# Kernel tuning notes

Measured on AMD Instinct MI355X. Metric: run time of the kernel, lower is better.

Reference implementation:

```python
import jax, jax.numpy as jnp
import numpy as np

NUM_LEVELS = 8
CODEBOOK_SIZE = 1024
EMBED_DIM = 256
BETA = 0.25
N_TOKENS = 65536
EPS = 1e-6


def setup_inputs() -> dict:
    key = jax.random.key(0)
    kz, kc = jax.random.split(key)
    z = jax.random.normal(kz, (N_TOKENS, EMBED_DIM), dtype=jnp.float32)
    # per-level init std = 1 / 2**i, matching nn.init.normal_ in __init__
    scales = (0.5 ** jnp.arange(NUM_LEVELS, dtype=jnp.float32))[:, None, None]
    codebooks = jax.random.normal(kc, (NUM_LEVELS, CODEBOOK_SIZE, EMBED_DIM), dtype=jnp.float32) * scales
    return {"z": z, "codebooks": codebooks}


def _normalize(v):
    # F.normalize(p=2, dim=-1, eps=1e-6): v / max(||v||, eps)
    return v / jnp.maximum(jnp.linalg.norm(v, axis=-1, keepdims=True), EPS)


def _rotation_trick(x, quantized):
    sg = jax.lax.stop_gradient
    u = _normalize(x)
    q = _normalize(quantized)
    w = _normalize(u + q)
    xw_dot = jnp.sum(x * sg(w), axis=-1, keepdims=True)
    xu_dot = jnp.sum(x * sg(u), axis=-1, keepdims=True)
    return x - 2.0 * xw_dot * sg(w) + 2.0 * xu_dot * sg(q)


def reference(z, codebooks):
    sg = jax.lax.stop_gradient
    residual = z
    quantized_sum = jnp.zeros_like(z)
    indices_list = []
    total_codebook_loss = jnp.float32(0.0)
    total_commitment_loss = jnp.float32(0.0)
    for lvl in range(NUM_LEVELS):
        c = codebooks[lvl]  # [K, D]
        # squared-euclidean distances up to constant ||x||^2 (argmin-equivalent, as in source)
        c_sq = jnp.sum(c * c, axis=1)                      # [K]
        dists = c_sq - 2.0 * (residual @ c.T)              # [N, K]
        min_idx = jnp.argmin(dists, axis=-1)               # [N]
        indices_list.append(min_idx)
        z_q_local = c[min_idx]                             # gather [N, D]
        total_codebook_loss = total_codebook_loss + jnp.mean((z_q_local - sg(residual)) ** 2)
        total_commitment_loss = total_commitment_loss + jnp.mean((sg(z_q_local) - residual) ** 2)
        # training path uses the rotation-trick estimator
        z_q_st = _rotation_trick(residual, z_q_local)
        residual = residual - z_q_st
        quantized_sum = quantized_sum + z_q_local
    indices = jnp.stack(indices_list, axis=-1)             # [N, L]
    loss = total_codebook_loss + BETA * total_commitment_loss
    # perplexity (codebook utilization entropy)
    flat = indices.reshape(-1)
    counts = jnp.zeros((CODEBOOK_SIZE,), jnp.float32).at[flat].add(1.0)
    probs = counts / jnp.float32(flat.size)
    safe = jnp.where(probs > 0, probs, 1.0)
    entropy = -jnp.sum(probs * jnp.log(safe))
    perplexity = jnp.exp(entropy)
    # straight-through output
    z_q = z + sg(quantized_sum - z)
    return (z_q, indices, loss, total_codebook_loss, total_commitment_loss, perplexity)
```

## Files before the change

### kernel.cpp

```cpp
#include <hip/hip_runtime.h>

#define N_TOK 65536
#define DIM 256
#define KCB 1024
#define NLVL 8
#define TPB 64
#define ND_OUT (N_TOK * DIM)
#define IDX_OFF ND_OUT
#define SC_OFF (ND_OUT + N_TOK * NLVL)
#define EPSV 1e-6f

typedef _Float16 half8 __attribute__((ext_vector_type(8)));
typedef float f32x4 __attribute__((ext_vector_type(4)));

__device__ __forceinline__ float wave_red(float v) {
    v += __shfl_xor(v, 32, 64);
    v += __shfl_xor(v, 16, 64);
    v += __shfl_xor(v, 8, 64);
    v += __shfl_xor(v, 4, 64);
    v += __shfl_xor(v, 2, 64);
    v += __shfl_xor(v, 1, 64);
    return v;
}

__device__ __forceinline__ unsigned int ordf(float d) {
    unsigned int u = __float_as_uint(d);
    return (u & 0x80000000u) ? ~u : (u ^ 0x80000000u);
}

__global__ __launch_bounds__(256) void k_prep(const float* __restrict__ cbs,
                                              half8* __restrict__ ws_b) {
    const int lvl = blockIdx.x >> 6, ntg = blockIdx.x & 63;
    const int lane = threadIdx.x & 63, sg = threadIdx.x >> 6;
    const float sc = (float)(1 << (lvl + 5));
#pragma unroll
    for (int ss = 0; ss < 2; ++ss) {
        const int s = sg + ss * 4;
        const int code = ntg * 16 + (lane & 15);
        const int d0 = s * 32 + (lane >> 4) * 8;
        const float* p = cbs + ((size_t)(lvl * KCB + code)) * DIM + d0;
        const float4 va = *(const float4*)p;
        const float4 vb = *(const float4*)(p + 4);
        float f[8] = {va.x, va.y, va.z, va.w, vb.x, vb.y, vb.z, vb.w};
        half8 h, l;
#pragma unroll
        for (int j = 0; j < 8; ++j) {
            float fs = f[j] * sc;
            _Float16 hh = (_Float16)fs;
            h[j] = hh;
            l[j] = (_Float16)(fs - (float)hh);
        }
        const size_t base = ((size_t)((lvl * 8 + s) * 64 + ntg)) * 128;
        ws_b[base + lane] = h;
        ws_b[base + 64 + lane] = l;
    }
}

__global__ __launch_bounds__(256) void k_csq(const float* __restrict__ cbs,
                                             float* __restrict__ csq_s,
                                             int* __restrict__ gcounts,
                                             float* __restrict__ gloss) {
    const int tid = threadIdx.x;
    const int wv = tid >> 6, lane = tid & 63;
    const int code = blockIdx.x * 4 + wv;
    const float4 v = *(const float4*)(cbs + (size_t)code * DIM + lane * 4);
    float s = v.x * v.x + v.y * v.y + v.z * v.z + v.w * v.w;
    s = wave_red(s);
    const int lvl = code >> 10;
    if (lane == 0) csq_s[code] = s * (float)(1 << (10 + lvl));
    if (blockIdx.x == 0) {
#pragma unroll
        for (int i = 0; i < 4; ++i) gcounts[tid + i * 256] = 0;
        if (tid == 0) *gloss = 0.f;
    }
}

__global__ __launch_bounds__(512, 2) void k_main(const float* __restrict__ z,
                                                 const float* __restrict__ cbs,
                                                 const half8* __restrict__ ws_b,
                                                 const float* __restrict__ csq_s,
                                                 float* __restrict__ out,
                                                 int* __restrict__ gcounts,
                                                 float* __restrict__ gloss) {
    __shared__ __align__(16) float Rld[TPB * DIM];
    __shared__ unsigned long long keyBuf[8][TPB];
    __shared__ int bestI_sh[TPB];
    __shared__ int idxBuf[TPB * NLVL];
    __shared__ int hist[KCB];
    __shared__ float wpart[8];

    const int tid = threadIdx.x;
    const int lane = tid & 63, w = tid >> 6;
    const int l15 = lane & 15, qd = lane >> 4;
    const int t0 = blockIdx.x * TPB;

#pragma unroll
    for (int i = 0; i < 8; ++i) {
        int fi = tid + i * 512;
        int t = fi >> 6, k4 = fi & 63;
        float4 v = *(const float4*)(z + (size_t)(t0 + t) * DIM + k4 * 4);
        v.x *= 32.f; v.y *= 32.f; v.z *= 32.f; v.w *= 32.f;
        *(float4*)&Rld[t * DIM + ((k4 ^ (t & 15)) << 2)] = v;
    }
#pragma unroll
    for (int i = 0; i < 2; ++i) hist[tid + i * 512] = 0;
    float loss_acc = 0.f;

    const half8* pbw = ws_b + (size_t)(w * 8) * 128 + lane;
    half8 bh = pbw[0], bl = pbw[64];
    __syncthreads();

    for (int lvl = 0; lvl < NLVL; ++lvl) {
        float bd[16];
        int bi[16];
#pragma unroll
        for (int i = 0; i < 16; ++i) { bd[i] = 3.402823466e38f; bi[i] = 0; }

        f32x4 acc[8][4];
#pragma unroll
        for (int nt = 0; nt < 8; ++nt)
#pragma unroll
            for (int m = 0; m < 4; ++m) acc[nt][m] = (f32x4){0.f, 0.f, 0.f, 0.f};

#pragma unroll 1
        for (int s = 0; s < 8; ++s) {
            half8 Ah[4], Al[4];
#pragma unroll
            for (int m = 0; m < 4; ++m) {
                const int row = (m * 16 + l15) * DIM;
                const int k4 = 8 * s + 2 * qd;
                float4 va = *(const float4*)&Rld[row + ((k4 ^ l15) << 2)];
                float4 vb = *(const float4*)&Rld[row + (((k4 + 1) ^ l15) << 2)];
                float f[8] = {va.x, va.y, va.z, va.w, vb.x, vb.y, vb.z, vb.w};
                half8 h, l;
#pragma unroll
                for (int j = 0; j < 8; ++j) {
                    _Float16 hh = (_Float16)f[j];
                    h[j] = hh;
                    l[j] = (_Float16)(f[j] - (float)hh);
                }
                Ah[m] = h;
                Al[m] = l;
            }
            const half8* pb = ws_b + (((size_t)(lvl * 8 + s)) * 64 + w * 8) * 128 + lane;
#pragma unroll
            for (int nt = 0; nt < 8; ++nt) {
                const int off = (nt < 7) ? (nt + 1) * 128 : 64 * 128;
                half8 nbh = pb[off];
                half8 nbl = pb[off + 64];
#pragma unroll
                for (int m = 0; m < 4; ++m)
                    acc[nt][m] = __builtin_amdgcn_mfma_f32_16x16x32_f16(Ah[m], bh, acc[nt][m], 0, 0, 0);
#pragma unroll
                for (int m = 0; m < 4; ++m)
                    acc[nt][m] = __builtin_amdgcn_mfma_f32_16x16x32_f16(Al[m], bh, acc[nt][m], 0, 0, 0);
#pragma unroll
                for (int m = 0; m < 4; ++m)
                    acc[nt][m] = __builtin_amdgcn_mfma_f32_16x16x32_f16(Ah[m], bl, acc[nt][m], 0, 0, 0);
#pragma unroll
                for (int m = 0; m < 4; ++m)
                    acc[nt][m] = __builtin_amdgcn_mfma_f32_16x16x32_f16(Al[m], bl, acc[nt][m], 0, 0, 0);
                bh = nbh;
                bl = nbl;
            }
        }
        {
            const float* csqp = csq_s + lvl * KCB + w * 128 + l15;
#pragma unroll
            for (int nt = 0; nt < 8; ++nt) {
                const float cs = csqp[nt * 16];
                const int code = w * 128 + nt * 16 + l15;
#pragma unroll
                for (int m = 0; m < 4; ++m)
#pragma unroll
                    for (int i = 0; i < 4; ++i) {
                        float d = fmaf(-2.f, acc[nt][m][i], cs);
                        if (d < bd[m * 4 + i]) { bd[m * 4 + i] = d; bi[m * 4 + i] = code; }
                    }
            }
        }
        unsigned long long key[16];
#pragma unroll
        for (int i = 0; i < 16; ++i)
            key[i] = (((unsigned long long)ordf(bd[i])) << 10) | (unsigned long long)bi[i];
#pragma unroll
        for (int m = 1; m <= 8; m <<= 1)
#pragma unroll
            for (int i = 0; i < 16; ++i) {
                unsigned long long o = __shfl_xor(key[i], m, 64);
                if (o < key[i]) key[i] = o;
            }
        if (l15 == 0) {
#pragma unroll
            for (int m = 0; m < 4; ++m)
#pragma unroll
                for (int i = 0; i < 4; ++i)
                    keyBuf[w][m * 16 + qd * 4 + i] = key[m * 4 + i];
        }
        __syncthreads();
        if (tid < TPB) {
            unsigned long long k = keyBuf[0][tid];
#pragma unroll
            for (int ww = 1; ww < 8; ++ww)
                if (keyBuf[ww][tid] < k) k = keyBuf[ww][tid];
            const int idx = (int)(k & 1023ull);
            bestI_sh[tid] = idx;
            idxBuf[tid * NLVL + lvl] = idx;
            atomicAdd(&hist[idx], 1);
        }
        __syncthreads();

        const float* cb = cbs + (size_t)lvl * KCB * DIM;
        for (int s2 = 0; s2 < 8; ++s2) {
            const int tl = w * 8 + s2;
            const int idx = bestI_sh[tl];
            const int e = tl & 15;
            float4 r4 = *(const float4*)&Rld[tl * DIM + ((lane ^ e) << 2)];
            r4.x *= 0.03125f; r4.y *= 0.03125f; r4.z *= 0.03125f; r4.w *= 0.03125f;
            float4 c4 = *(const float4*)(cb + (size_t)idx * DIM + lane * 4);
            float rr = r4.x * r4.x + r4.y * r4.y + r4.z * r4.z + r4.w * r4.w;
            float cc = c4.x * c4.x + c4.y * c4.y + c4.z * c4.z + c4.w * c4.w;
            float e0 = (c4.x - r4.x) * (c4.x - r4.x) + (c4.y - r4.y) * (c4.y - r4.y) +
                       (c4.z - r4.z) * (c4.z - r4.z) + (c4.w - r4.w) * (c4.w - r4.w);
            rr = wave_red(rr);
            cc = wave_red(cc);
            e0 = wave_red(e0);
            const float dx = fmaxf(sqrtf(rr), EPSV);
            const float dc = fmaxf(sqrtf(cc), EPSV);
            float4 u4 = make_float4(r4.x / dx, r4.y / dx, r4.z / dx, r4.w / dx);
            float4 q4 = make_float4(c4.x / dc, c4.y / dc, c4.z / dc, c4.w / dc);
            float4 w4 = make_float4(u4.x + q4.x, u4.y + q4.y, u4.z + q4.z, u4.w + q4.w);
            float ww = w4.x * w4.x + w4.y * w4.y + w4.z * w4.z + w4.w * w4.w;
            float xw = r4.x * w4.x + r4.y * w4.y + r4.z * w4.z + r4.w * w4.w;
            float xu = r4.x * u4.x + r4.y * u4.y + r4.z * u4.z + r4.w * u4.w;
            ww = wave_red(ww);
            xw = wave_red(xw);
            xu = wave_red(xu);
            const float dw = fmaxf(sqrtf(ww), EPSV);
            const float xwn = xw / dw;
            float4 wn = make_float4(w4.x / dw, w4.y / dw, w4.z / dw, w4.w / dw);
            float4 zst = make_float4(r4.x - 2.f * xwn * wn.x + 2.f * xu * q4.x,
                                     r4.y - 2.f * xwn * wn.y + 2.f * xu * q4.y,
                                     r4.z - 2.f * xwn * wn.z + 2.f * xu * q4.z,
                                     r4.w - 2.f * xwn * wn.w + 2.f * xu * q4.w);
            float4 rn = make_float4((r4.x - zst.x) * 32.f, (r4.y - zst.y) * 32.f,
                                    (r4.z - zst.z) * 32.f, (r4.w - zst.w) * 32.f);
            *(float4*)&Rld[tl * DIM + ((lane ^ e) << 2)] = rn;
            loss_acc += e0;
        }
        __syncthreads();
    }

    for (int s2 = 0; s2 < 8; ++s2) {
        const int tl = w * 8 + s2;
        const size_t trow = t0 + tl;
        float4 z4 = *(const float4*)(z + trow * DIM + lane * 4);
        float4 qs = make_float4(0.f, 0.f, 0.f, 0.f);
#pragma unroll
        for (int lvl = 0; lvl < NLVL; ++lvl) {
            const int idx = idxBuf[tl * NLVL + lvl];
            float4 c4 = *(const float4*)(cbs + ((size_t)(lvl * KCB + idx)) * DIM + lane * 4);
            qs.x += c4.x; qs.y += c4.y; qs.z += c4.z; qs.w += c4.w;
        }
        float4 o = make_float4(z4.x + (qs.x - z4.x), z4.y + (qs.y - z4.y),
                               z4.z + (qs.z - z4.z), z4.w + (qs.w - z4.w));
        *(float4*)(out + trow * DIM + lane * 4) = o;
    }
    out[IDX_OFF + (size_t)(t0 + (tid >> 3)) * NLVL + (tid & 7)] = (float)idxBuf[tid];
#pragma unroll
    for (int i = 0; i < 2; ++i) {
        int b = tid + i * 512;
        int h = hist[b];
        if (h) atomicAdd(&gcounts[b], h);
    }
    if (lane == 0) wpart[w] = loss_acc;
    __syncthreads();
    if (tid == 0) {
        float sum = 0.f;
#pragma unroll
        for (int i = 0; i < 8; ++i) sum += wpart[i];
        atomicAdd(gloss, sum);
    }
}

__global__ __launch_bounds__(256) void k_fin(const int* __restrict__ gcounts,
                                             const float* __restrict__ gloss,
                                             float* __restrict__ out) {
    __shared__ float part[4];
    const int tid = threadIdx.x, lane = tid & 63, wv = tid >> 6;
    float e = 0.f;
#pragma unroll
    for (int i = 0; i < 4; ++i) {
        float c = (float)gcounts[tid * 4 + i];
        float p = c * (1.f / 524288.f);
        if (p > 0.f) e += p * logf(p);
    }
    e = wave_red(e);
    if (lane == 0) part[wv] = e;
    __syncthreads();
    if (tid == 0) {
        float ent = -(part[0] + part[1] + part[2] + part[3]);
        float cbl = *gloss * (1.f / 16777216.f);
        out[SC_OFF + 0] = cbl + 0.25f * cbl;
        out[SC_OFF + 1] = cbl;
        out[SC_OFF + 2] = cbl;
        out[SC_OFF + 3] = expf(ent);
    }
}

extern "C" void kernel_launch(void* const* d_in, const int* in_sizes, int n_in,
                              void* d_out, int out_size, void* d_ws, size_t ws_size,
                              hipStream_t stream) {
    (void)in_sizes; (void)n_in; (void)out_size; (void)ws_size;
    const float* z = (const float*)d_in[0];
    const float* cbs = (const float*)d_in[1];
    float* out = (float*)d_out;
    half8* ws_b = (half8*)d_ws;
    float* csq = (float*)((char*)d_ws + (8u << 20));
    int* gcounts = (int*)((char*)d_ws + (8u << 20) + 32768);
    float* gloss = (float*)((char*)d_ws + (8u << 20) + 32768 + 4096);

    hipLaunchKernelGGL(k_prep, dim3(512), dim3(256), 0, stream, cbs, ws_b);
    hipLaunchKernelGGL(k_csq, dim3(2048), dim3(256), 0, stream, cbs, csq, gcounts, gloss);
    hipLaunchKernelGGL(k_main, dim3(1024), dim3(512), 0, stream, z, cbs, ws_b, csq, out,
                       gcounts, gloss);
    hipLaunchKernelGGL(k_fin, dim3(1), dim3(256), 0, stream, gcounts, gloss, out);
}
```

Measured before the change: 1.355 ms.

## Precompute split-fp16 A fragments in LDS once per level and use per-wave argmin reduce

Each level now converts the residual tile into hi/lo fp16 MFMA fragments once into shared memory, instead of every wave redoing the conversion in the inner loop. The cross-wave argmin reduction is done per wave via shuffles, removing a barrier and the bestI buffer. This cuts redundant VALU conversion work and one sync. In exchange it adds 64KB of LDS, which may reduce blocks per CU, and an extra barrier before the matmul.

```diff
diff --git a/kernel.cpp b/kernel.cpp
--- a/kernel.cpp
+++ b/kernel.cpp
@@ -83,8 +83,8 @@
                                                  int* __restrict__ gcounts,
                                                  float* __restrict__ gloss) {
     __shared__ __align__(16) float Rld[TPB * DIM];
-    __shared__ unsigned long long keyBuf[8][TPB];
-    __shared__ int bestI_sh[TPB];
+    __shared__ __align__(16) half8 Afrag[4096];
+    __shared__ unsigned long long keyBuf[8][TPB + 1];
     __shared__ int idxBuf[TPB * NLVL];
     __shared__ int hist[KCB];
     __shared__ float wpart[8];
@@ -111,6 +111,29 @@
     __syncthreads();
 
     for (int lvl = 0; lvl < NLVL; ++lvl) {
+#pragma unroll
+        for (int i = 0; i < 4; ++i) {
+            const int f = tid + i * 512;
+            const int sm = f >> 6, ln = f & 63;
+            const int s = sm >> 2, m = sm & 3;
+            const int e = ln & 15;
+            const int row = (m * 16 + e) * DIM;
+            const int k4 = s * 8 + ((ln >> 4) << 1);
+            float4 va = *(const float4*)&Rld[row + ((k4 ^ e) << 2)];
+            float4 vb = *(const float4*)&Rld[row + (((k4 + 1) ^ e) << 2)];
+            float fv[8] = {va.x, va.y, va.z, va.w, vb.x, vb.y, vb.z, vb.w};
+            half8 h, l;
+#pragma unroll
+            for (int j = 0; j < 8; ++j) {
+                _Float16 hh = (_Float16)fv[j];
+                h[j] = hh;
+                l[j] = (_Float16)(fv[j] - (float)hh);
+            }
+            Afrag[sm * 128 + ln] = h;
+            Afrag[sm * 128 + 64 + ln] = l;
+        }
+        __syncthreads();
+
         float bd[16];
         int bi[16];
 #pragma unroll
@@ -127,20 +150,8 @@
             half8 Ah[4], Al[4];
 #pragma unroll
             for (int m = 0; m < 4; ++m) {
-                const int row = (m * 16 + l15) * DIM;
-                const int k4 = 8 * s + 2 * qd;
-                float4 va = *(const float4*)&Rld[row + ((k4 ^ l15) << 2)];
-                float4 vb = *(const float4*)&Rld[row + (((k4 + 1) ^ l15) << 2)];
-                float f[8] = {va.x, va.y, va.z, va.w, vb.x, vb.y, vb.z, vb.w};
-                half8 h, l;
-#pragma unroll
-                for (int j = 0; j < 8; ++j) {
-                    _Float16 hh = (_Float16)f[j];
-                    h[j] = hh;
-                    l[j] = (_Float16)(f[j] - (float)hh);
-                }
-                Ah[m] = h;
-                Al[m] = l;
+                Ah[m] = Afrag[(s * 4 + m) * 128 + lane];
+                Al[m] = Afrag[(s * 4 + m) * 128 + 64 + lane];
             }
             const half8* pb = ws_b + (((size_t)(lvl * 8 + s)) * 64 + w * 8) * 128 + lane;
 #pragma unroll
@@ -198,22 +209,23 @@
                     keyBuf[w][m * 16 + qd * 4 + i] = key[m * 4 + i];
         }
         __syncthreads();
-        if (tid < TPB) {
-            unsigned long long k = keyBuf[0][tid];
-#pragma unroll
-            for (int ww = 1; ww < 8; ++ww)
-                if (keyBuf[ww][tid] < k) k = keyBuf[ww][tid];
-            const int idx = (int)(k & 1023ull);
-            bestI_sh[tid] = idx;
-            idxBuf[tid * NLVL + lvl] = idx;
-            atomicAdd(&hist[idx], 1);
-        }
-        __syncthreads();
+        unsigned long long kk = keyBuf[lane & 7][w * 8 + (lane >> 3)];
+        {
+            unsigned long long o1 = __shfl_xor(kk, 1, 64); if (o1 < kk) kk = o1;
+            unsigned long long o2 = __shfl_xor(kk, 2, 64); if (o2 < kk) kk = o2;
+            unsigned long long o4 = __shfl_xor(kk, 4, 64); if (o4 < kk) kk = o4;
+        }
+        const int myidx = (int)(kk & 1023ull);
+        if ((lane & 7) == 0) {
+            const int tl = w * 8 + (lane >> 3);
+            idxBuf[tl * NLVL + lvl] = myidx;
+            atomicAdd(&hist[myidx], 1);
+        }
 
         const float* cb = cbs + (size_t)lvl * KCB * DIM;
         for (int s2 = 0; s2 < 8; ++s2) {
             const int tl = w * 8 + s2;
-            const int idx = bestI_sh[tl];
+            const int idx = __shfl(myidx, s2 * 8, 64);
             const int e = tl & 15;
             float4 r4 = *(const float4*)&Rld[tl * DIM + ((lane ^ e) << 2)];
             r4.x *= 0.03125f; r4.y *= 0.03125f; r4.z *= 0.03125f; r4.w *= 0.03125f;
```

Result: faster. 1.256 ms (-7.3%).
